# Kernel tuning notes

Hardware: AMD Instinct MI355X
Metric: run time of the kernel (lower is better)

The kernel has to match this reference:

```python
import jax, jax.numpy as jnp
import numpy as np

K_HOPS = 2  # num_layers in NewSGConv


def setup_inputs() -> dict:
    key = jax.random.key(0)
    ks = jax.random.split(key, 5)
    B, N, F, H, C = 2048, 64, 256, 512, 2
    n_tril = N * (N + 1) // 2  # 2080
    X = jax.random.normal(ks[0], (B, N, F), dtype=jnp.float32)
    edge_weight_tril = jax.random.normal(ks[1], (n_tril,), dtype=jnp.float32) * 0.1
    conv_W = jax.random.normal(ks[2], (F, H), dtype=jnp.float32) * (1.0 / np.sqrt(F))
    conv_b = jnp.zeros((H,), dtype=jnp.float32)
    fc_W = jax.random.normal(ks[3], (C, H), dtype=jnp.float32) * (1.0 / np.sqrt(H))
    fc_b = jnp.zeros((C,), dtype=jnp.float32)
    return {"X": X, "edge_weight_tril": edge_weight_tril, "conv_W": conv_W,
            "conv_b": conv_b, "fc_W": fc_W, "fc_b": fc_b}


def reference(X, edge_weight_tril, conv_W, conv_b, fc_W, fc_b):
    # X: [B, N, F] ; graph is fully connected over N nodes, shared across batch.
    N = X.shape[1]
    xs, ys = jnp.tril_indices(N)
    # Rebuild symmetric dense weight matrix from lower-triangular learnable params
    W = jnp.zeros((N, N), dtype=X.dtype).at[xs, ys].set(edge_weight_tril)
    W = W + W.T - jnp.diag(jnp.diag(W))
    # NewSGConv norm: add self-loops (fill=1), deg from abs(edge_weight)
    A = W + jnp.eye(N, dtype=X.dtype)                 # W_sym + I (extra self-loop edge)
    deg = jnp.abs(W).sum(axis=1) + 1.0                # abs of self-loop weight = 1
    dinv = jnp.where(deg > 0, deg ** -0.5, 0.0)
    An = dinv[:, None] * A * dinv[None, :]            # D^-1/2 (W_sym + I) D^-1/2
    # K-hop SGConv propagation (dense graph -> batched matmul is the exact math)
    x = X
    for _ in range(K_HOPS):
        x = jnp.einsum('nm,bmf->bnf', An, x)
    # SGConv linear, then ReLU (as in model forward)
    h = jax.nn.relu(jnp.einsum('bnf,fh->bnh', x, conv_W) + conv_b)  # [B,N,H]
    # global_add_pool over nodes per graph
    pooled = h.sum(axis=1)                            # [B, H]
    # dropout is identity in eval; final fc + log_softmax
    logits = pooled @ fc_W.T + fc_b                   # [B, C]
    return jax.nn.log_softmax(logits, axis=-1)
```

## Files before the change

### kernel.cpp

```cpp
#include <hip/hip_runtime.h>

typedef float f32x4 __attribute__((ext_vector_type(4)));
typedef short bf16x8 __attribute__((ext_vector_type(8)));

__device__ __forceinline__ short f2bf(float x) {
    unsigned u = __float_as_uint(x);
    unsigned r = (u + 0x7FFFu + ((u >> 16) & 1u)) >> 16;
    return (short)r;
}

__global__ void prep_an2(const float* __restrict__ tril, short* __restrict__ an2f) {
    __shared__ float Wm[64][64];
    __shared__ float An[64][64];
    __shared__ float An2[64][64];
    __shared__ float dinv[64];
    const int t = threadIdx.x;
    for (int e = t; e < 4096; e += 256) {
        int i = e >> 6, j = e & 63;
        int hi = i > j ? i : j, lo = i > j ? j : i;
        Wm[i][j] = tril[hi * (hi + 1) / 2 + lo];
    }
    __syncthreads();
    if (t < 64) {
        float s = 0.f;
        for (int j = 0; j < 64; ++j) s += fabsf(Wm[t][j]);
        s += 1.0f;
        dinv[t] = (s > 0.f) ? 1.0f / sqrtf(s) : 0.f;
    }
    __syncthreads();
    for (int e = t; e < 4096; e += 256) {
        int i = e >> 6, j = e & 63;
        float a = Wm[i][j] + (i == j ? 1.0f : 0.0f);
        An[i][j] = dinv[i] * a * dinv[j];
    }
    __syncthreads();
    for (int e = t; e < 4096; e += 256) {
        int i = e >> 6, j = e & 63;
        float acc = 0.f;
        for (int m = 0; m < 64; ++m) acc += An[i][m] * An[m][j];
        An2[i][j] = acc;
    }
    __syncthreads();
    for (int o = t; o < 4096; o += 256) {
        int e = o & 7, lane = (o >> 3) & 63, kt = (o >> 9) & 1, mt = o >> 10;
        int m = mt * 16 + (lane & 15);
        int k = kt * 32 + 8 * (lane >> 4) + e;
        an2f[o] = f2bf(An2[m][k]);
    }
}

__global__ void prep_wf(const float* __restrict__ convW, short* __restrict__ wf) {
    int o = blockIdx.x * 256 + threadIdx.x;
    int e = o & 7, lane = (o >> 3) & 63, nt = (o >> 9) & 31, kt = o >> 14;
    int k = kt * 32 + 8 * (lane >> 4) + e;
    int j = nt * 16 + (lane & 15);
    wf[o] = f2bf(convW[k * 512 + j]);
}

__global__ __launch_bounds__(256, 2) void rgnn_main(
    const float* __restrict__ X, const short* __restrict__ an2f,
    const short* __restrict__ wf, const float* __restrict__ convb,
    const float* __restrict__ fcW, const float* __restrict__ fcb,
    float* __restrict__ out)
{
    __shared__ short xbt[256 * 64];
    __shared__ short xs[64 * 256];
    __shared__ float pooled[512];
    const int b = blockIdx.x;
    const int t = threadIdx.x;
    const int lane = t & 63;
    const int wid = t >> 6;
    const float* Xb = X + (size_t)b * (64 * 256);

    {
        const int c = t;
        #pragma unroll
        for (int m0 = 0; m0 < 64; m0 += 8) {
            bf16x8 v;
            #pragma unroll
            for (int i = 0; i < 8; ++i) v[i] = f2bf(Xb[(m0 + i) * 256 + c]);
            int byte = c * 128 + m0 * 2;
            byte ^= (c & 7) << 4;
            *(bf16x8*)((char*)xbt + byte) = v;
        }
    }
    __syncthreads();

    {
        const int c0 = wid * 64;
        f32x4 acc[4][4];
        #pragma unroll
        for (int mt = 0; mt < 4; ++mt)
            #pragma unroll
            for (int nt = 0; nt < 4; ++nt) acc[mt][nt] = (f32x4)0.f;
        bf16x8 afr[4][2];
        #pragma unroll
        for (int mt = 0; mt < 4; ++mt)
            #pragma unroll
            for (int kt = 0; kt < 2; ++kt)
                afr[mt][kt] = *(const bf16x8*)&an2f[((mt * 2 + kt) * 64 + lane) * 8];
        #pragma unroll
        for (int kt = 0; kt < 2; ++kt) {
            #pragma unroll
            for (int nt = 0; nt < 4; ++nt) {
                int row = c0 + nt * 16 + (lane & 15);
                int byte = row * 128 + (kt * 32 + 8 * (lane >> 4)) * 2;
                byte ^= (row & 7) << 4;
                bf16x8 bfr = *(const bf16x8*)((const char*)xbt + byte);
                #pragma unroll
                for (int mt = 0; mt < 4; ++mt)
                    acc[mt][nt] = __builtin_amdgcn_mfma_f32_16x16x32_bf16(afr[mt][kt], bfr, acc[mt][nt], 0, 0, 0);
            }
        }
        #pragma unroll
        for (int mt = 0; mt < 4; ++mt)
            #pragma unroll
            for (int nt = 0; nt < 4; ++nt)
                #pragma unroll
                for (int r = 0; r < 4; ++r) {
                    int row = mt * 16 + (lane >> 4) * 4 + r;
                    int col = c0 + nt * 16 + (lane & 15);
                    int byte = row * 512 + col * 2;
                    byte ^= (row & 7) << 4;
                    *(short*)((char*)xs + byte) = f2bf(acc[mt][nt][r]);
                }
    }
    __syncthreads();

    {
        const int j0 = wid * 128;
        f32x4 acc[4][8];
        #pragma unroll
        for (int mt = 0; mt < 4; ++mt)
            #pragma unroll
            for (int nt = 0; nt < 8; ++nt) acc[mt][nt] = (f32x4)0.f;
        #pragma unroll
        for (int kt = 0; kt < 8; ++kt) {
            bf16x8 bfr[8];
            #pragma unroll
            for (int nt = 0; nt < 8; ++nt) {
                int ntg = (j0 >> 4) + nt;
                bfr[nt] = *(const bf16x8*)&wf[((kt * 32 + ntg) * 64 + lane) * 8];
            }
            #pragma unroll
            for (int mt = 0; mt < 4; ++mt) {
                int row = mt * 16 + (lane & 15);
                int byte = row * 512 + (kt * 32 + 8 * (lane >> 4)) * 2;
                byte ^= (row & 7) << 4;
                bf16x8 afr = *(const bf16x8*)((const char*)xs + byte);
                #pragma unroll
                for (int nt = 0; nt < 8; ++nt)
                    acc[mt][nt] = __builtin_amdgcn_mfma_f32_16x16x32_bf16(afr, bfr[nt], acc[mt][nt], 0, 0, 0);
            }
        }
        #pragma unroll
        for (int nt = 0; nt < 8; ++nt) {
            int j = j0 + nt * 16 + (lane & 15);
            float bj = convb[j];
            float s = 0.f;
            #pragma unroll
            for (int mt = 0; mt < 4; ++mt)
                #pragma unroll
                for (int r = 0; r < 4; ++r)
                    s += fmaxf(acc[mt][nt][r] + bj, 0.f);
            s += __shfl_xor(s, 16);
            s += __shfl_xor(s, 32);
            if (lane < 16) pooled[j] = s;
        }
    }
    __syncthreads();

    if (wid == 0) {
        float p0 = 0.f, p1 = 0.f;
        #pragma unroll
        for (int j = lane; j < 512; j += 64) {
            float pv = pooled[j];
            p0 += pv * fcW[j];
            p1 += pv * fcW[512 + j];
        }
        #pragma unroll
        for (int d = 1; d < 64; d <<= 1) {
            p0 += __shfl_xor(p0, d);
            p1 += __shfl_xor(p1, d);
        }
        if (lane == 0) {
            float l0 = p0 + fcb[0], l1 = p1 + fcb[1];
            float m = fmaxf(l0, l1);
            float lse = m + logf(expf(l0 - m) + expf(l1 - m));
            out[b * 2 + 0] = l0 - lse;
            out[b * 2 + 1] = l1 - lse;
        }
    }
}

extern "C" void kernel_launch(void* const* d_in, const int* in_sizes, int n_in,
                              void* d_out, int out_size, void* d_ws, size_t ws_size,
                              hipStream_t stream) {
    const float* X     = (const float*)d_in[0];
    const float* tril  = (const float*)d_in[1];
    const float* convW = (const float*)d_in[2];
    const float* convb = (const float*)d_in[3];
    const float* fcW   = (const float*)d_in[4];
    const float* fcb   = (const float*)d_in[5];
    float* out = (float*)d_out;
    short* an2f = (short*)d_ws;
    short* wf   = an2f + 4096;
    prep_an2<<<dim3(1), dim3(256), 0, stream>>>(tril, an2f);
    prep_wf<<<dim3(512), dim3(256), 0, stream>>>(convW, wf);
    rgnn_main<<<dim3(2048), dim3(256), 0, stream>>>(X, an2f, wf, convb, fcW, fcb, out);
}
```

Baseline: 89.90 us.

## Load X directly into MFMA fragments, drop transpose LDS buffer, raise occupancy

Removes the 32KB shared-memory transposed copy of X and its barrier, so each wave reads X from global memory straight into bf16 B-fragments for the propagation matmul. The second GEMM is split into two sequential halves of 64 columns to halve the accumulator registers, and launch bounds go from 2 to 4 blocks per CU. The aim is lower LDS and register use, giving more resident blocks to hide memory latency. The cost is strided, less coalesced global reads of X (each lane reads 8 floats 256 apart) and the wf fragments being loaded twice per k-step across the halves.

```diff
diff --git a/kernel.cpp b/kernel.cpp
--- a/kernel.cpp
+++ b/kernel.cpp
@@ -57,13 +57,12 @@
     wf[o] = f2bf(convW[k * 512 + j]);
 }
 
-__global__ __launch_bounds__(256, 2) void rgnn_main(
+__global__ __launch_bounds__(256, 4) void rgnn_main(
     const float* __restrict__ X, const short* __restrict__ an2f,
     const short* __restrict__ wf, const float* __restrict__ convb,
     const float* __restrict__ fcW, const float* __restrict__ fcb,
     float* __restrict__ out)
 {
-    __shared__ short xbt[256 * 64];
     __shared__ short xs[64 * 256];
     __shared__ float pooled[512];
     const int b = blockIdx.x;
@@ -73,44 +72,31 @@
     const float* Xb = X + (size_t)b * (64 * 256);
 
     {
-        const int c = t;
-        #pragma unroll
-        for (int m0 = 0; m0 < 64; m0 += 8) {
-            bf16x8 v;
-            #pragma unroll
-            for (int i = 0; i < 8; ++i) v[i] = f2bf(Xb[(m0 + i) * 256 + c]);
-            int byte = c * 128 + m0 * 2;
-            byte ^= (c & 7) << 4;
-            *(bf16x8*)((char*)xbt + byte) = v;
-        }
-    }
-    __syncthreads();
-
-    {
         const int c0 = wid * 64;
         f32x4 acc[4][4];
         #pragma unroll
         for (int mt = 0; mt < 4; ++mt)
             #pragma unroll
             for (int nt = 0; nt < 4; ++nt) acc[mt][nt] = (f32x4)0.f;
-        bf16x8 afr[4][2];
-        #pragma unroll
-        for (int mt = 0; mt < 4; ++mt)
-            #pragma unroll
-            for (int kt = 0; kt < 2; ++kt)
-                afr[mt][kt] = *(const bf16x8*)&an2f[((mt * 2 + kt) * 64 + lane) * 8];
         #pragma unroll
         for (int kt = 0; kt < 2; ++kt) {
+            bf16x8 bfr[4];
             #pragma unroll
             for (int nt = 0; nt < 4; ++nt) {
-                int row = c0 + nt * 16 + (lane & 15);
-                int byte = row * 128 + (kt * 32 + 8 * (lane >> 4)) * 2;
-                byte ^= (row & 7) << 4;
-                bf16x8 bfr = *(const bf16x8*)((const char*)xbt + byte);
+                const int cc = c0 + nt * 16 + (lane & 15);
+                const float* src = Xb + (kt * 32 + 8 * (lane >> 4)) * 256 + cc;
                 #pragma unroll
-                for (int mt = 0; mt < 4; ++mt)
-                    acc[mt][nt] = __builtin_amdgcn_mfma_f32_16x16x32_bf16(afr[mt][kt], bfr, acc[mt][nt], 0, 0, 0);
+                for (int e = 0; e < 8; ++e) bfr[nt][e] = f2bf(src[e * 256]);
             }
+            bf16x8 afr[4];
+            #pragma unroll
+            for (int mt = 0; mt < 4; ++mt)
+                afr[mt] = *(const bf16x8*)&an2f[((mt * 2 + kt) * 64 + lane) * 8];
+            #pragma unroll
+            for (int mt = 0; mt < 4; ++mt)
+                #pragma unroll
+                for (int nt = 0; nt < 4; ++nt)
+                    acc[mt][nt] = __builtin_amdgcn_mfma_f32_16x16x32_bf16(afr[mt], bfr[nt], acc[mt][nt], 0, 0, 0);
         }
         #pragma unroll
         for (int mt = 0; mt < 4; ++mt)
@@ -127,18 +113,19 @@
     }
     __syncthreads();
 
-    {
-        const int j0 = wid * 128;
-        f32x4 acc[4][8];
+    #pragma unroll 1
+    for (int half = 0; half < 2; ++half) {
+        const int j0 = wid * 128 + half * 64;
+        f32x4 acc[4][4];
         #pragma unroll
         for (int mt = 0; mt < 4; ++mt)
             #pragma unroll
-            for (int nt = 0; nt < 8; ++nt) acc[mt][nt] = (f32x4)0.f;
+            for (int nt = 0; nt < 4; ++nt) acc[mt][nt] = (f32x4)0.f;
         #pragma unroll
         for (int kt = 0; kt < 8; ++kt) {
-            bf16x8 bfr[8];
+            bf16x8 bfr[4];
             #pragma unroll
-            for (int nt = 0; nt < 8; ++nt) {
+            for (int nt = 0; nt < 4; ++nt) {
                 int ntg = (j0 >> 4) + nt;
                 bfr[nt] = *(const bf16x8*)&wf[((kt * 32 + ntg) * 64 + lane) * 8];
             }
@@ -149,12 +136,12 @@
                 byte ^= (row & 7) << 4;
                 bf16x8 afr = *(const bf16x8*)((const char*)xs + byte);
                 #pragma unroll
-                for (int nt = 0; nt < 8; ++nt)
+                for (int nt = 0; nt < 4; ++nt)
                     acc[mt][nt] = __builtin_amdgcn_mfma_f32_16x16x32_bf16(afr, bfr[nt], acc[mt][nt], 0, 0, 0);
             }
         }
         #pragma unroll
-        for (int nt = 0; nt < 8; ++nt) {
+        for (int nt = 0; nt < 4; ++nt) {
             int j = j0 + nt * 16 + (lane & 15);
             float bj = convb[j];
             float s = 0.f;
```

Result: slower. 197.0 us (+119.2%).

## Stage X tile into LDS via async global_load_lds and convert to bf16 on read

Applied to the files above, without the earlier changes.

Replaces the per-thread strided fp32 loads and bf16 transpose-store of X with direct global-to-LDS 16-byte async copies into a 64KB fp32 buffer. The XOR swizzle is applied on the source address, and the bf16 conversion happens when the first GEMM's B fragments are read from LDS. The An² fragment loads are hoisted so they overlap the async copy, and an extra barrier lets the fp32 buffer be reused for the intermediate result. The goal is to cut global-load instruction overhead and register traffic. In exchange the block now uses about 66KB of LDS instead of 64KB plus pooled, which may reduce occupancy from two blocks per CU, and the B-fragment reads become scalar 4-byte LDS loads.

```diff
diff --git a/kernel.cpp b/kernel.cpp
--- a/kernel.cpp
+++ b/kernel.cpp
@@ -1,4 +1,5 @@
 #include <hip/hip_runtime.h>
+#include <hip/hip_bf16.h>
 
 typedef float f32x4 __attribute__((ext_vector_type(4)));
 typedef short bf16x8 __attribute__((ext_vector_type(8)));
@@ -7,6 +8,12 @@
     unsigned u = __float_as_uint(x);
     unsigned r = (u + 0x7FFFu + ((u >> 16) & 1u)) >> 16;
     return (short)r;
+}
+
+__device__ __forceinline__ void gld_lds16(const void* g, void* l) {
+    __builtin_amdgcn_global_load_lds(
+        (const __attribute__((address_space(1))) unsigned int*)g,
+        (__attribute__((address_space(3))) unsigned int*)l, 16, 0, 0);
 }
 
 __global__ void prep_an2(const float* __restrict__ tril, short* __restrict__ an2f) {
@@ -63,9 +70,9 @@
     const float* __restrict__ fcW, const float* __restrict__ fcb,
     float* __restrict__ out)
 {
-    __shared__ short xbt[256 * 64];
-    __shared__ short xs[64 * 256];
+    __shared__ char smem[65536];
     __shared__ float pooled[512];
+    short* xs = (short*)smem;
     const int b = blockIdx.x;
     const int t = threadIdx.x;
     const int lane = t & 63;
@@ -73,45 +80,53 @@
     const float* Xb = X + (size_t)b * (64 * 256);
 
     {
-        const int c = t;
-        #pragma unroll
-        for (int m0 = 0; m0 < 64; m0 += 8) {
-            bf16x8 v;
-            #pragma unroll
-            for (int i = 0; i < 8; ++i) v[i] = f2bf(Xb[(m0 + i) * 256 + c]);
-            int byte = c * 128 + m0 * 2;
-            byte ^= (c & 7) << 4;
-            *(bf16x8*)((char*)xbt + byte) = v;
-        }
-    }
-    __syncthreads();
-
+        const char* XbB = (const char*)Xb;
+        #pragma unroll
+        for (int i = 0; i < 16; ++i) {
+            const int chunk = wid * 16 + i;
+            const int key = (chunk >> 3) & 3;
+            gld_lds16(XbB + chunk * 1024 + ((lane ^ (key << 1)) * 16), smem + chunk * 1024);
+        }
+    }
+    bf16x8 afr[4][2];
+    #pragma unroll
+    for (int mt = 0; mt < 4; ++mt)
+        #pragma unroll
+        for (int kt = 0; kt < 2; ++kt)
+            afr[mt][kt] = *(const bf16x8*)&an2f[((mt * 2 + kt) * 64 + lane) * 8];
+    __syncthreads();
+
+    f32x4 acc_a[4][4];
     {
         const int c0 = wid * 64;
-        f32x4 acc[4][4];
         #pragma unroll
         for (int mt = 0; mt < 4; ++mt)
             #pragma unroll
-            for (int nt = 0; nt < 4; ++nt) acc[mt][nt] = (f32x4)0.f;
-        bf16x8 afr[4][2];
-        #pragma unroll
-        for (int mt = 0; mt < 4; ++mt)
-            #pragma unroll
-            for (int kt = 0; kt < 2; ++kt)
-                afr[mt][kt] = *(const bf16x8*)&an2f[((mt * 2 + kt) * 64 + lane) * 8];
+            for (int nt = 0; nt < 4; ++nt) acc_a[mt][nt] = (f32x4)0.f;
         #pragma unroll
         for (int kt = 0; kt < 2; ++kt) {
+            bf16x8 bfr[4];
             #pragma unroll
             for (int nt = 0; nt < 4; ++nt) {
-                int row = c0 + nt * 16 + (lane & 15);
-                int byte = row * 128 + (kt * 32 + 8 * (lane >> 4)) * 2;
-                byte ^= (row & 7) << 4;
-                bf16x8 bfr = *(const bf16x8*)((const char*)xbt + byte);
-                #pragma unroll
-                for (int mt = 0; mt < 4; ++mt)
-                    acc[mt][nt] = __builtin_amdgcn_mfma_f32_16x16x32_bf16(afr[mt][kt], bfr, acc[mt][nt], 0, 0, 0);
+                const int cc = c0 + nt * 16 + (lane & 15);
+                #pragma unroll
+                for (int e = 0; e < 8; ++e) {
+                    const int m = kt * 32 + 8 * (lane >> 4) + e;
+                    const int a = ((m * 1024 + cc * 4) ^ ((lane >> 4) << 5));
+                    bfr[nt][e] = f2bf(*(const float*)(smem + a));
+                }
             }
-        }
+            #pragma unroll
+            for (int mt = 0; mt < 4; ++mt)
+                #pragma unroll
+                for (int nt = 0; nt < 4; ++nt)
+                    acc_a[mt][nt] = __builtin_amdgcn_mfma_f32_16x16x32_bf16(afr[mt][kt], bfr[nt], acc_a[mt][nt], 0, 0, 0);
+        }
+    }
+    __syncthreads();
+
+    {
+        const int c0 = wid * 64;
         #pragma unroll
         for (int mt = 0; mt < 4; ++mt)
             #pragma unroll
@@ -122,7 +137,7 @@
                     int col = c0 + nt * 16 + (lane & 15);
                     int byte = row * 512 + col * 2;
                     byte ^= (row & 7) << 4;
-                    *(short*)((char*)xs + byte) = f2bf(acc[mt][nt][r]);
+                    *(short*)((char*)xs + byte) = f2bf(acc_a[mt][nt][r]);
                 }
     }
     __syncthreads();
@@ -147,10 +162,10 @@
                 int row = mt * 16 + (lane & 15);
                 int byte = row * 512 + (kt * 32 + 8 * (lane >> 4)) * 2;
                 byte ^= (row & 7) << 4;
-                bf16x8 afr = *(const bf16x8*)((const char*)xs + byte);
+                bf16x8 afrb = *(const bf16x8*)((const char*)xs + byte);
                 #pragma unroll
                 for (int nt = 0; nt < 8; ++nt)
-                    acc[mt][nt] = __builtin_amdgcn_mfma_f32_16x16x32_bf16(afr, bfr[nt], acc[mt][nt], 0, 0, 0);
+                    acc[mt][nt] = __builtin_amdgcn_mfma_f32_16x16x32_bf16(afrb, bfr[nt], acc[mt][nt], 0, 0, 0);
             }
         }
         #pragma unroll
```

Result: no change. 90.22 us (+0.4%).
